# Kernel optimization log

Measured on AMD Instinct MI355X. Metric: run time of the kernel, lower is better.

The kernel has to match this reference:

```python
import jax, jax.numpy as jnp
import numpy as np

# Water box constants: n_atoms=192 -> 64 oxygens (type 8) + 128 hydrogens (type 1)
N_O, N_H = 64, 128
XLIM = 6.0  # params.max_rdf_dist


def _hist(d, bins):
    """np.histogram-equivalent fixed-bin histogram of 1-D values d."""
    nb = bins.shape[0] - 1
    idx = jnp.clip(jnp.searchsorted(bins, d, side='right') - 1, 0, nb - 1)
    w = ((d >= bins[0]) & (d <= bins[-1])).astype(jnp.float32)
    return jnp.zeros((nb,), jnp.float32).at[idx].add(w)


def _pair_rdf(wrapped, idx0, idx1, lattices, bins):
    # wrapped: [T, N, 3]; replicates distance_pbc_select + histogram/RDF math
    x0 = wrapped[:, idx0]                       # [T, n0, 3] (type1 atoms)
    x1 = wrapped[:, idx1]                       # [T, n1, 3] (type2 atoms)
    # x0.repeat([1,n1,1]) vs x1.repeat_interleave(n0) == outer pairing (x1 outer, x0 inner)
    delta = jnp.abs(x0[:, None, :, :] - x1[:, :, None, :])   # [T, n1, n0, 3]
    delta = jnp.where(delta > 0.5 * lattices, delta - lattices, delta)
    s = (delta ** 2).sum(-1)                    # [T, n1, n0]
    # safe sqrt (self-pairs give exact zeros)
    d = jnp.where(s > 0, jnp.sqrt(jnp.where(s > 0, s, 1.0)), 0.0)
    T = d.shape[0]
    P = d.shape[1] * d.shape[2]
    d = d.reshape(T, P)
    hists = jax.vmap(lambda dd: _hist(dd, bins))(d)          # [T, nb]
    vol = jnp.prod(lattices)
    shell = (4.0 / 3.0) * jnp.pi * (bins[1:] ** 3 - bins[:-1] ** 3)
    # aggregate RDF over all frames (zeros fall below bins[0]=1e-6, excluded)
    Z1 = (T * P / vol) * shell
    data_rdf = hists.sum(0) / Z1
    # per-frame RDFs, renormalized to the aggregate RDF's total mass
    Z2 = (T / vol) * shell
    rdfs = hists / Z2
    rdfs = rdfs / rdfs.sum(1, keepdims=True) * data_rdf.sum()
    return rdfs.mean(0)                          # [nb]


def setup_inputs() -> dict:
    key = jax.random.key(0)
    k0, k1, k2, k3 = jax.random.split(key, 4)
    T, R, N, nb = 100, 8, 192, 600
    stacked_radii = jax.random.normal(k0, (T, R, N, 3), jnp.float32) * 5.0
    ptypes = jnp.tile(jnp.array([8, 1, 1], jnp.int32), N // 3)  # O,H,H per water
    lattices = jnp.full((3,), 12.42, jnp.float32)
    bins = jnp.asarray(np.linspace(1e-6, XLIM, nb + 1), jnp.float32)
    gt_oo = jax.random.uniform(k1, (1, nb), jnp.float32)
    gt_hh = jax.random.uniform(k2, (1, nb), jnp.float32)
    gt_ho = jax.random.uniform(k3, (1, nb), jnp.float32)
    return dict(stacked_radii=stacked_radii, ptypes=ptypes, lattices=lattices,
                bins=bins, gt_oo=gt_oo, gt_hh=gt_hh, gt_ho=gt_ho)


def reference(stacked_radii, ptypes, lattices, bins, gt_oo, gt_hh, gt_ho):
    idx_O = jnp.nonzero(ptypes == 8, size=N_O)[0]
    idx_H = jnp.nonzero(ptypes == 1, size=N_H)[0]

    def per_replica(data):                       # data: [T, N, 3]
        wrapped = data / lattices % 1 * lattices  # PBC wrap into box
        rdf_oo = _pair_rdf(wrapped, idx_O, idx_O, lattices, bins)
        rdf_hh = _pair_rdf(wrapped, idx_H, idx_H, lattices, bins)
        rdf_ho = _pair_rdf(wrapped, idx_H, idx_O, lattices, bins)
        maes = jnp.stack([
            XLIM * jnp.abs(rdf_oo[None] - gt_oo).mean(),
            XLIM * jnp.abs(rdf_hh[None] - gt_hh).mean(),
            XLIM * jnp.abs(rdf_ho[None] - gt_ho).mean(),
        ])
        return jnp.concatenate([rdf_oo, rdf_hh, rdf_ho]), maes.max()

    # [T, R, N, 3] -> [R, T, N, 3], vmap over replicas
    rdf_list, max_maes = jax.vmap(per_replica)(jnp.swapaxes(stacked_radii, 0, 1))
    return rdf_list, max_maes
```

## Files before the change

### kernel.cpp

```cpp
#include <hip/hip_runtime.h>

#define T_STEPS 100
#define R_REP   8
#define N_ATOMS 192
#define NBINS   600

__global__ __launch_bounds__(256) void rdf_hist_kernel(
    const float* __restrict__ radii,
    const float* __restrict__ lattices,
    const float* __restrict__ bins,
    float* __restrict__ hist_out,
    float* __restrict__ sigma_out)
{
#pragma clang fp contract(off)
    __shared__ float    Tq[NBINS + 2];
    __shared__ unsigned shist[4][NBINS];
    __shared__ float4   sA[128];
    __shared__ float4   sB[64];
    __shared__ float    sred[256];

    const int blk = blockIdx.x;
    const int p   = blk % 3;
    const int t   = (blk / 3) % T_STEPS;
    const int r   = blk / (3 * T_STEPS);
    const int tid = threadIdx.x;

    for (int b = tid; b <= NBINS + 1; b += 256) {
        if (b <= NBINS) {
            float e = bins[b];
            unsigned u = __float_as_uint(e * e);
            while (sqrtf(__uint_as_float(u)) <  e) ++u;
            while (sqrtf(__uint_as_float(u - 1)) >= e) --u;
            Tq[b] = __uint_as_float(u);
        } else {
            unsigned u = __float_as_uint(36.0f);
            while (sqrtf(__uint_as_float(u)) <= 6.0f) ++u;
            while (sqrtf(__uint_as_float(u - 1)) > 6.0f) --u;
            Tq[NBINS + 1] = __uint_as_float(u);
        }
    }
    for (int b = tid; b < NBINS; b += 256) {
        shist[0][b] = 0u; shist[1][b] = 0u; shist[2][b] = 0u; shist[3][b] = 0u;
    }

    const float L0 = lattices[0], L1 = lattices[1], L2 = lattices[2];
    const float* base = radii + (size_t)(t * R_REP + r) * (N_ATOMS * 3);

    auto load_set = [&](float4* dst, int n, bool isH) {
#pragma clang fp contract(off)
        for (int a = tid; a < n; a += 256) {
            int atom = isH ? (3 * (a >> 1) + 1 + (a & 1)) : (3 * a);
            const float* src = base + atom * 3;
            float x = src[0], y = src[1], z = src[2];
            float qx = x / L0; float wx = (qx - floorf(qx)) * L0;
            float qy = y / L1; float wy = (qy - floorf(qy)) * L1;
            float qz = z / L2; float wz = (qz - floorf(qz)) * L2;
            dst[a] = make_float4(wx, wy, wz, 0.0f);
        }
    };

    if (p == 0)      { load_set(sA, 64, false); }
    else if (p == 1) { load_set(sA, 128, true); }
    else             { load_set(sA, 128, true); load_set(sB, 64, false); }
    __syncthreads();

    const float T0 = Tq[0];
    const float TG = Tq[NBINS + 1];
    const float b0f = bins[0];
    const float invstep = (float)NBINS / (6.0f - b0f);
    const float h0 = 0.5f * L0, h1 = 0.5f * L1, h2 = 0.5f * L2;
    unsigned* myh = shist[tid >> 6];

    auto bin_pair = [&](float4 A, float4 B, unsigned w) {
#pragma clang fp contract(off)
        float dx = fabsf(A.x - B.x); dx = fminf(dx, fabsf(dx - L0));
        float dy = fabsf(A.y - B.y); dy = fminf(dy, fabsf(dy - L1));
        float dz = fabsf(A.z - B.z); dz = fminf(dz, fabsf(dz - L2));
        float s = dx * dx + dy * dy + dz * dz;
        if (s < T0 || s >= TG) return;
        float dhat = __builtin_amdgcn_sqrtf(s);
        int k0 = (int)((dhat - b0f) * invstep);
        if (k0 > NBINS - 1) k0 = NBINS - 1;
        float lo = Tq[k0], hi = Tq[k0 + 1];
        int bi = k0 + (int)(s >= hi) - (int)(s < lo);
        if (bi > NBINS - 1) bi = NBINS - 1;
        atomicAdd(&myh[bi], w);
    };

    if (p == 2) {
        float4 A = sA[tid & 127];
        int jbase = (tid >> 7);
#pragma unroll
        for (int it = 0; it < 32; ++it)
            bin_pair(A, sB[jbase + it * 2], 1u);
    } else if (p == 1) {
        int i = tid & 127;
        float4 A = sA[i];
        int kbase = (tid >> 7) + 1;
#pragma unroll
        for (int it = 0; it < 32; ++it) {
            int k = kbase + it * 2;
            bin_pair(A, sA[(i + k) & 127], (k == 64) ? 1u : 2u);
        }
    } else {
        int i = tid & 63;
        float4 A = sA[i];
        int kbase = (tid >> 6) + 1;
#pragma unroll
        for (int it = 0; it < 8; ++it) {
            int k = kbase + it * 4;
            bin_pair(A, sA[(i + k) & 63], (k == 32) ? 1u : 2u);
        }
    }
    __syncthreads();

    float* outp = hist_out + (size_t)((r * 3 + p) * T_STEPS + t) * NBINS;
    float lsig = 0.0f;
    for (int b = tid; b < NBINS; b += 256) {
        float fc = (float)(shist[0][b] + shist[1][b] + shist[2][b] + shist[3][b]);
        outp[b] = fc;
        float e0 = bins[b], e1 = bins[b + 1];
        float shell = 4.18879020478639053f * (e1 * e1 * e1 - e0 * e0 * e0);
        lsig += fc / shell;
    }
    sred[tid] = lsig;
    __syncthreads();
    for (int s2 = 128; s2 > 0; s2 >>= 1) {
        if (tid < s2) sred[tid] += sred[tid + s2];
        __syncthreads();
    }
    if (tid == 0) sigma_out[(r * 3 + p) * T_STEPS + t] = sred[0];
}

__global__ __launch_bounds__(640) void rdf_norm_kernel(
    const float* __restrict__ hist,
    const float* __restrict__ sigma,
    const float* __restrict__ bins,
    const float* __restrict__ lattices,
    const float* __restrict__ gt_oo,
    const float* __restrict__ gt_hh,
    const float* __restrict__ gt_ho,
    float* __restrict__ out)
{
#pragma clang fp contract(off)
    __shared__ float ssig[T_STEPS];
    __shared__ float sinvsig[T_STEPS];
    __shared__ float sred[640];
    __shared__ float sS;

    const int blk = blockIdx.x;
    const int p = blk % 3, r = blk / 3;
    const int tid = threadIdx.x;
    const float* h = hist + (size_t)blk * T_STEPS * NBINS;

    if (tid < T_STEPS) {
        float sg = sigma[blk * T_STEPS + tid];
        ssig[tid] = sg;
        sinvsig[tid] = 1.0f / sg;
    }
    __syncthreads();
    if (tid == 0) {
        float s = 0.0f;
        for (int t = 0; t < T_STEPS; ++t) s += ssig[t];
        float vol = lattices[0] * lattices[1] * lattices[2];
        float Pf = (p == 0) ? 4096.0f : ((p == 1) ? 16384.0f : 8192.0f);
        sS = vol / ((float)T_STEPS * Pf) * s;
    }
    __syncthreads();

    const float S = sS;
    const float* gt = (p == 0) ? gt_oo : ((p == 1) ? gt_hh : gt_ho);
    float lacc = 0.0f;
    const int b = tid;
    if (b < NBINS) {
        float a0 = 0.0f, a1 = 0.0f, a2 = 0.0f, a3 = 0.0f;
        const float* hb = h + b;
        for (int t = 0; t < T_STEPS; t += 4) {
            a0 += hb[(t + 0) * NBINS] * sinvsig[t + 0];
            a1 += hb[(t + 1) * NBINS] * sinvsig[t + 1];
            a2 += hb[(t + 2) * NBINS] * sinvsig[t + 2];
            a3 += hb[(t + 3) * NBINS] * sinvsig[t + 3];
        }
        float e0 = bins[b], e1 = bins[b + 1];
        float shell = 4.18879020478639053f * (e1 * e1 * e1 - e0 * e0 * e0);
        float v = S * (1.0f / (float)T_STEPS) * (1.0f / shell) * ((a0 + a1) + (a2 + a3));
        out[r * 1800 + p * 600 + b] = v;
        lacc = fabsf(v - gt[b]);
    }
    sred[tid] = lacc;
    __syncthreads();
    for (int s2 = 512; s2 > 0; s2 >>= 1) {
        if (tid < s2 && tid + s2 < 640) sred[tid] += sred[tid + s2];
        __syncthreads();
    }
    if (tid == 0) {
        float mae = 6.0f * (sred[0] / 600.0f);
        atomicMax((int*)&out[14400 + r], __float_as_int(mae));
    }
}

extern "C" void kernel_launch(void* const* d_in, const int* in_sizes, int n_in,
                              void* d_out, int out_size, void* d_ws, size_t ws_size,
                              hipStream_t stream) {
    const float* radii    = (const float*)d_in[0];
    const float* lattices = (const float*)d_in[2];
    const float* bins     = (const float*)d_in[3];
    const float* gt_oo    = (const float*)d_in[4];
    const float* gt_hh    = (const float*)d_in[5];
    const float* gt_ho    = (const float*)d_in[6];
    float* out = (float*)d_out;

    float* hist  = (float*)d_ws;
    float* sigma = hist + (size_t)R_REP * 3 * T_STEPS * NBINS;

    hipLaunchKernelGGL(rdf_hist_kernel, dim3(R_REP * 3 * T_STEPS), dim3(256), 0, stream,
                       radii, lattices, bins, hist, sigma);
    hipLaunchKernelGGL(rdf_norm_kernel, dim3(R_REP * 3), dim3(640), 0, stream,
                       hist, sigma, bins, lattices, gt_oo, gt_hh, gt_ho, out);
}
```

Measured before the change: 92.38 us.

## Fuse pair types per frame block and accumulate normalized histograms atomically

Each block now processes one (time, replica) frame and computes all three pair-type histograms, loading the atom coordinates once instead of three times. Blocks normalize each frame's histogram by its own sigma and atomically add it into a small per-replica accumulator in global memory, so the large per-frame histogram buffer and its readback in the final kernel go away. This adds a memset launch, global float atomics whose summation order is nondeterministic, and more shared memory per block.

```diff
diff --git a/kernel.cpp b/kernel.cpp
--- a/kernel.cpp
+++ b/kernel.cpp
@@ -2,28 +2,27 @@
 
 #define T_STEPS 100
 #define R_REP   8
-#define N_ATOMS 192
 #define NBINS   600
 
-__global__ __launch_bounds__(256) void rdf_hist_kernel(
+__global__ __launch_bounds__(256) void rdf_fused_kernel(
     const float* __restrict__ radii,
     const float* __restrict__ lattices,
     const float* __restrict__ bins,
-    float* __restrict__ hist_out,
-    float* __restrict__ sigma_out)
+    float* __restrict__ acc,
+    float* __restrict__ sigsum)
 {
 #pragma clang fp contract(off)
     __shared__ float    Tq[NBINS + 2];
-    __shared__ unsigned shist[4][NBINS];
-    __shared__ float4   sA[128];
-    __shared__ float4   sB[64];
-    __shared__ float    sred[256];
+    __shared__ unsigned hist3[3][4][NBINS];
+    __shared__ float4   sH[128];
+    __shared__ float4   sO[64];
+    __shared__ float    sredw[4][3];
+    __shared__ float    sInv[3];
 
     const int blk = blockIdx.x;
-    const int p   = blk % 3;
-    const int t   = (blk / 3) % T_STEPS;
-    const int r   = blk / (3 * T_STEPS);
+    const int r   = blk % R_REP;
     const int tid = threadIdx.x;
+    const int wid = tid >> 6;
 
     for (int b = tid; b <= NBINS + 1; b += 256) {
         if (b <= NBINS) {
@@ -39,39 +38,34 @@
             Tq[NBINS + 1] = __uint_as_float(u);
         }
     }
-    for (int b = tid; b < NBINS; b += 256) {
-        shist[0][b] = 0u; shist[1][b] = 0u; shist[2][b] = 0u; shist[3][b] = 0u;
+    {
+        uint4* z = (uint4*)&hist3[0][0][0];
+        for (int k = tid; k < 1800; k += 256) z[k] = make_uint4(0u, 0u, 0u, 0u);
     }
 
     const float L0 = lattices[0], L1 = lattices[1], L2 = lattices[2];
-    const float* base = radii + (size_t)(t * R_REP + r) * (N_ATOMS * 3);
-
-    auto load_set = [&](float4* dst, int n, bool isH) {
-#pragma clang fp contract(off)
-        for (int a = tid; a < n; a += 256) {
-            int atom = isH ? (3 * (a >> 1) + 1 + (a & 1)) : (3 * a);
-            const float* src = base + atom * 3;
-            float x = src[0], y = src[1], z = src[2];
-            float qx = x / L0; float wx = (qx - floorf(qx)) * L0;
-            float qy = y / L1; float wy = (qy - floorf(qy)) * L1;
-            float qz = z / L2; float wz = (qz - floorf(qz)) * L2;
-            dst[a] = make_float4(wx, wy, wz, 0.0f);
-        }
-    };
-
-    if (p == 0)      { load_set(sA, 64, false); }
-    else if (p == 1) { load_set(sA, 128, true); }
-    else             { load_set(sA, 128, true); load_set(sB, 64, false); }
+    const float* base = radii + (size_t)blk * 576;
+
+    if (tid < 192) {
+        int isH  = (tid >= 64);
+        int a    = isH ? (tid - 64) : tid;
+        int atom = isH ? (3 * (a >> 1) + 1 + (a & 1)) : (3 * a);
+        const float* src = base + atom * 3;
+        float x = src[0], y = src[1], z = src[2];
+        float qx = x / L0; float wx = (qx - floorf(qx)) * L0;
+        float qy = y / L1; float wy = (qy - floorf(qy)) * L1;
+        float qz = z / L2; float wz = (qz - floorf(qz)) * L2;
+        float4 w4 = make_float4(wx, wy, wz, 0.0f);
+        if (isH) sH[a] = w4; else sO[a] = w4;
+    }
     __syncthreads();
 
     const float T0 = Tq[0];
     const float TG = Tq[NBINS + 1];
     const float b0f = bins[0];
     const float invstep = (float)NBINS / (6.0f - b0f);
-    const float h0 = 0.5f * L0, h1 = 0.5f * L1, h2 = 0.5f * L2;
-    unsigned* myh = shist[tid >> 6];
-
-    auto bin_pair = [&](float4 A, float4 B, unsigned w) {
+
+    auto bin_pair = [&](unsigned* myh, float4 A, float4 B, unsigned w) {
 #pragma clang fp contract(off)
         float dx = fabsf(A.x - B.x); dx = fminf(dx, fabsf(dx - L0));
         float dy = fabsf(A.y - B.y); dy = fminf(dy, fabsf(dy - L1));
@@ -87,54 +81,90 @@
         atomicAdd(&myh[bi], w);
     };
 
-    if (p == 2) {
-        float4 A = sA[tid & 127];
-        int jbase = (tid >> 7);
-#pragma unroll
-        for (int it = 0; it < 32; ++it)
-            bin_pair(A, sB[jbase + it * 2], 1u);
-    } else if (p == 1) {
+    unsigned* mOO = hist3[0][wid];
+    unsigned* mHH = hist3[1][wid];
+    unsigned* mHO = hist3[2][wid];
+    {
+        int i = tid & 63;
+        int kbase = (tid >> 6) + 1;
+        float4 A = sO[i];
+#pragma unroll
+        for (int it = 0; it < 8; ++it) {
+            int k = kbase + it * 4;
+            bin_pair(mOO, A, sO[(i + k) & 63], (k == 32) ? 1u : 2u);
+        }
+    }
+    {
         int i = tid & 127;
-        float4 A = sA[i];
         int kbase = (tid >> 7) + 1;
+        float4 A = sH[i];
 #pragma unroll
         for (int it = 0; it < 32; ++it) {
             int k = kbase + it * 2;
-            bin_pair(A, sA[(i + k) & 127], (k == 64) ? 1u : 2u);
-        }
-    } else {
-        int i = tid & 63;
-        float4 A = sA[i];
-        int kbase = (tid >> 6) + 1;
-#pragma unroll
-        for (int it = 0; it < 8; ++it) {
-            int k = kbase + it * 4;
-            bin_pair(A, sA[(i + k) & 63], (k == 32) ? 1u : 2u);
-        }
-    }
-    __syncthreads();
-
-    float* outp = hist_out + (size_t)((r * 3 + p) * T_STEPS + t) * NBINS;
-    float lsig = 0.0f;
-    for (int b = tid; b < NBINS; b += 256) {
-        float fc = (float)(shist[0][b] + shist[1][b] + shist[2][b] + shist[3][b]);
-        outp[b] = fc;
-        float e0 = bins[b], e1 = bins[b + 1];
-        float shell = 4.18879020478639053f * (e1 * e1 * e1 - e0 * e0 * e0);
-        lsig += fc / shell;
-    }
-    sred[tid] = lsig;
-    __syncthreads();
-    for (int s2 = 128; s2 > 0; s2 >>= 1) {
-        if (tid < s2) sred[tid] += sred[tid + s2];
-        __syncthreads();
-    }
-    if (tid == 0) sigma_out[(r * 3 + p) * T_STEPS + t] = sred[0];
+            bin_pair(mHH, A, sH[(i + k) & 127], (k == 64) ? 1u : 2u);
+        }
+        int jb = tid >> 7;
+#pragma unroll
+        for (int it = 0; it < 32; ++it)
+            bin_pair(mHO, A, sO[jb + it * 2], 1u);
+    }
+    __syncthreads();
+
+    float fcs[3][3];
+    float invsh[3];
+    float lsig0 = 0.0f, lsig1 = 0.0f, lsig2 = 0.0f;
+#pragma unroll
+    for (int ii = 0; ii < 3; ++ii) {
+        int b = tid + ii * 256;
+        if (b < NBINS) {
+            float e0 = bins[b], e1 = bins[b + 1];
+            float shell = 4.18879020478639053f * (e1 * e1 * e1 - e0 * e0 * e0);
+            float is = 1.0f / shell;
+            invsh[ii] = is;
+            float f0 = (float)(hist3[0][0][b] + hist3[0][1][b] + hist3[0][2][b] + hist3[0][3][b]);
+            float f1 = (float)(hist3[1][0][b] + hist3[1][1][b] + hist3[1][2][b] + hist3[1][3][b]);
+            float f2 = (float)(hist3[2][0][b] + hist3[2][1][b] + hist3[2][2][b] + hist3[2][3][b]);
+            fcs[ii][0] = f0; fcs[ii][1] = f1; fcs[ii][2] = f2;
+            lsig0 += f0 * is; lsig1 += f1 * is; lsig2 += f2 * is;
+        } else {
+            fcs[ii][0] = 0.0f; fcs[ii][1] = 0.0f; fcs[ii][2] = 0.0f;
+            invsh[ii] = 0.0f;
+        }
+    }
+#pragma unroll
+    for (int off = 32; off > 0; off >>= 1) {
+        lsig0 += __shfl_down(lsig0, off, 64);
+        lsig1 += __shfl_down(lsig1, off, 64);
+        lsig2 += __shfl_down(lsig2, off, 64);
+    }
+    if ((tid & 63) == 0) {
+        sredw[wid][0] = lsig0; sredw[wid][1] = lsig1; sredw[wid][2] = lsig2;
+    }
+    __syncthreads();
+    if (tid < 3) {
+        float sg = sredw[0][tid] + sredw[1][tid] + sredw[2][tid] + sredw[3][tid];
+        sInv[tid] = 1.0f / sg;
+        atomicAdd(&sigsum[r * 3 + tid], sg);
+    }
+    __syncthreads();
+
+    const float i0 = sInv[0], i1 = sInv[1], i2 = sInv[2];
+    float* accr = acc + (size_t)r * 3 * NBINS;
+#pragma unroll
+    for (int ii = 0; ii < 3; ++ii) {
+        int b = tid + ii * 256;
+        if (b < NBINS) {
+            float f0 = fcs[ii][0], f1 = fcs[ii][1], f2 = fcs[ii][2];
+            if (f0 != 0.0f) atomicAdd(&accr[0 * NBINS + b], f0 * i0);
+            if (f1 != 0.0f) atomicAdd(&accr[1 * NBINS + b], f1 * i1);
+            if (f2 != 0.0f) atomicAdd(&accr[2 * NBINS + b], f2 * i2);
+        }
+    }
 }
 
-__global__ __launch_bounds__(640) void rdf_norm_kernel(
-    const float* __restrict__ hist,
-    const float* __restrict__ sigma,
+__global__ __launch_bounds__(640) void rdf_final_kernel(
+    const float* __restrict__ acc,
+    const float* __restrict__ sigsum,
     const float* __restrict__ bins,
     const float* __restrict__ lattices,
     const float* __restrict__ gt_oo,
@@ -143,49 +173,24 @@
     float* __restrict__ out)
 {
 #pragma clang fp contract(off)
-    __shared__ float ssig[T_STEPS];
-    __shared__ float sinvsig[T_STEPS];
     __shared__ float sred[640];
-    __shared__ float sS;
 
     const int blk = blockIdx.x;
     const int p = blk % 3, r = blk / 3;
     const int tid = threadIdx.x;
-    const float* h = hist + (size_t)blk * T_STEPS * NBINS;
-
-    if (tid < T_STEPS) {
-        float sg = sigma[blk * T_STEPS + tid];
-        ssig[tid] = sg;
-        sinvsig[tid] = 1.0f / sg;
-    }
-    __syncthreads();
-    if (tid == 0) {
-        float s = 0.0f;
-        for (int t = 0; t < T_STEPS; ++t) s += ssig[t];
-        float vol = lattices[0] * lattices[1] * lattices[2];
-        float Pf = (p == 0) ? 4096.0f : ((p == 1) ? 16384.0f : 8192.0f);
-        sS = vol / ((float)T_STEPS * Pf) * s;
-    }
-    __syncthreads();
-
-    const float S = sS;
+
+    const float vol = lattices[0] * lattices[1] * lattices[2];
+    const float Pf  = (p == 0) ? 4096.0f : ((p == 1) ? 16384.0f : 8192.0f);
+    const float S   = vol / ((float)T_STEPS * Pf) * sigsum[blk];
+
     const float* gt = (p == 0) ? gt_oo : ((p == 1) ? gt_hh : gt_ho);
     float lacc = 0.0f;
-    const int b = tid;
-    if (b < NBINS) {
-        float a0 = 0.0f, a1 = 0.0f, a2 = 0.0f, a3 = 0.0f;
-        const float* hb = h + b;
-        for (int t = 0; t < T_STEPS; t += 4) {
-            a0 += hb[(t + 0) * NBINS] * sinvsig[t + 0];
-            a1 += hb[(t + 1) * NBINS] * sinvsig[t + 1];
-            a2 += hb[(t + 2) * NBINS] * sinvsig[t + 2];
-            a3 += hb[(t + 3) * NBINS] * sinvsig[t + 3];
-        }
-        float e0 = bins[b], e1 = bins[b + 1];
+    if (tid < NBINS) {
+        float e0 = bins[tid], e1 = bins[tid + 1];
         float shell = 4.18879020478639053f * (e1 * e1 * e1 - e0 * e0 * e0);
-        float v = S * (1.0f / (float)T_STEPS) * (1.0f / shell) * ((a0 + a1) + (a2 + a3));
-        out[r * 1800 + p * 600 + b] = v;
-        lacc = fabsf(v - gt[b]);
+        float v = S * (1.0f / (float)T_STEPS) * (1.0f / shell) * acc[blk * NBINS + tid];
+        out[r * 1800 + p * 600 + tid] = v;
+        lacc = fabsf(v - gt[tid]);
     }
     sred[tid] = lacc;
     __syncthreads();
@@ -210,11 +215,13 @@
     const float* gt_ho    = (const float*)d_in[6];
     float* out = (float*)d_out;
 
-    float* hist  = (float*)d_ws;
-    float* sigma = hist + (size_t)R_REP * 3 * T_STEPS * NBINS;
-
-    hipLaunchKernelGGL(rdf_hist_kernel, dim3(R_REP * 3 * T_STEPS), dim3(256), 0, stream,
-                       radii, lattices, bins, hist, sigma);
-    hipLaunchKernelGGL(rdf_norm_kernel, dim3(R_REP * 3), dim3(640), 0, stream,
-                       hist, sigma, bins, lattices, gt_oo, gt_hh, gt_ho, out);
+    float* acc    = (float*)d_ws;
+    float* sigsum = acc + 24 * NBINS;
+
+    hipMemsetAsync(d_ws, 0, (24 * NBINS + 24) * sizeof(float), stream);
+
+    hipLaunchKernelGGL(rdf_fused_kernel, dim3(T_STEPS * R_REP), dim3(256), 0, stream,
+                       radii, lattices, bins, acc, sigsum);
+    hipLaunchKernelGGL(rdf_final_kernel, dim3(24), dim3(640), 0, stream,
+                       acc, sigsum, bins, lattices, gt_oo, gt_hh, gt_ho, out);
 }
```

After: 93.98 us. About the same (+1.7%).
